# Optimization experiments

Measured on AMD Instinct MI355X. Metric: run time of the kernel, lower is better.

Reference implementation:

```python
import jax, jax.numpy as jnp
import numpy as np
import math

MASK_FILL = -1e6  # d2l masked_softmax fills masked scores with -1e6


def setup_inputs() -> dict:
    key = jax.random.key(0)
    kq, kk, kv, kl = jax.random.split(key, 4)
    B, Lq, Lk, D = 16, 2048, 2048, 64
    queries = jax.random.normal(kq, (B, Lq, D), dtype=jnp.float32)
    keys = jax.random.normal(kk, (B, Lk, D), dtype=jnp.float32)
    values = jax.random.normal(kv, (B, Lk, D), dtype=jnp.float32)
    valid_lens = jax.random.randint(kl, (B,), 1, Lk + 1, dtype=jnp.int32)
    return {"queries": queries, "keys": keys, "values": values, "valid_lens": valid_lens}


def reference(queries, keys, values, valid_lens):
    # scores: [B, Lq, Lk]
    d = queries.shape[-1]
    scores = jnp.einsum("bqd,bkd->bqk", queries, keys) / math.sqrt(d)
    # masked_softmax: positions >= valid_lens[b] along key axis get -1e6
    Lk = keys.shape[1]
    mask = jnp.arange(Lk)[None, None, :] < valid_lens[:, None, None]  # [B,1,Lk]
    scores = jnp.where(mask, scores, MASK_FILL)
    attn = jax.nn.softmax(scores, axis=-1)
    # dropout p=0.0 (eval) is identity
    return jnp.einsum("bqk,bkd->bqd", attn, values)
```

## Files before the change

kernel.cpp:

```cpp
#include <hip/hip_runtime.h>
#include <hip/hip_bf16.h>
#include <stdint.h>


#define BATCH 16
#define SEQ   2048
#define DIM   64
#define KBLK  32
#define QBLK  64
#define NSPLIT 2
#define NTHR  256

typedef __bf16 bf16x8 __attribute__((ext_vector_type(8)));
typedef float  f32x16 __attribute__((ext_vector_type(16)));
typedef unsigned int u32x2 __attribute__((ext_vector_type(2)));

static constexpr float QSCALE = 0.125f * 1.44269504088896340736f;

__device__ __forceinline__ uint32_t pk2bf(float a, float b) {
    union { __hip_bfloat162 h; uint32_t u; } c;
    c.h = __float22bfloat162_rn(make_float2(a, b));
    return c.u;
}
__device__ __forceinline__ bf16x8 mk8(uint32_t w0, uint32_t w1, uint32_t w2, uint32_t w3) {
    union { uint32_t u[4]; bf16x8 v; } c;
    c.u[0] = w0; c.u[1] = w1; c.u[2] = w2; c.u[3] = w3;
    return c.v;
}
__device__ __forceinline__ u32x2 plswap(uint32_t a, uint32_t b) {
    return __builtin_amdgcn_permlane32_swap(a, b, false, false);
}
__device__ __forceinline__ float vmax16(const f32x16& v) {
    float a = fmaxf(fmaxf(v[0], v[1]), fmaxf(v[2], v[3]));
    float b = fmaxf(fmaxf(v[4], v[5]), fmaxf(v[6], v[7]));
    float c = fmaxf(fmaxf(v[8], v[9]), fmaxf(v[10], v[11]));
    float d = fmaxf(fmaxf(v[12], v[13]), fmaxf(v[14], v[15]));
    return fmaxf(fmaxf(a, b), fmaxf(c, d));
}
__device__ __forceinline__ float vsum16(const f32x16& v) {
    float a = (v[0] + v[1]) + (v[2] + v[3]);
    float b = (v[4] + v[5]) + (v[6] + v[7]);
    float c = (v[8] + v[9]) + (v[10] + v[11]);
    float d = (v[12] + v[13]) + (v[14] + v[15]);
    return (a + b) + (c + d);
}

__global__ __launch_bounds__(256) void prep_kv(
        const float* __restrict__ K, const float* __restrict__ V,
        unsigned short* __restrict__ Kbf, unsigned short* __restrict__ Vt)
{
    __shared__ float tl[64][65];
    const int bid = blockIdx.x;
    const int b  = bid >> 5;
    const int kb = (bid & 31) * 64;
    const int tid = threadIdx.x;

    const float* Kp = K + ((size_t)b * SEQ + kb) * DIM;
    const float* Vp = V + ((size_t)b * SEQ + kb) * DIM;
    unsigned short* Ko = Kbf + ((size_t)b * SEQ + kb) * DIM;
    unsigned short* Vo = Vt + (size_t)b * SEQ * DIM + (size_t)(kb >> 5) * 2048;

    #pragma unroll
    for (int p = 0; p < 4; ++p) {
        int idx = p * 256 + tid;
        float4 x = ((const float4*)Kp)[idx];
        ((uint2*)Ko)[idx] = make_uint2(pk2bf(x.x, x.y), pk2bf(x.z, x.w));
    }
    #pragma unroll
    for (int p = 0; p < 4; ++p) {
        int idx = p * 256 + tid;
        int r = idx >> 4, c = (idx & 15) * 4;
        float4 x = *(const float4*)(Vp + r * DIM + c);
        tl[r][c] = x.x; tl[r][c+1] = x.y; tl[r][c+2] = x.z; tl[r][c+3] = x.w;
    }
    __syncthreads();
    #pragma unroll
    for (int p = 0; p < 4; ++p) {
        int idx = p * 256 + tid;
        int sub = idx >> 9;
        int rem = idx & 511;
        int d  = rem >> 3;
        int kq = (rem & 7) * 4;
        int kr = sub * 32 + kq;
        *(uint2*)(Vo + sub * 2048 + d * 32 + kq) =
            make_uint2(pk2bf(tl[kr][d],     tl[kr + 1][d]),
                       pk2bf(tl[kr + 2][d], tl[kr + 3][d]));
    }
}

__global__ __launch_bounds__(NTHR, 2) void attn_main(
        const float* __restrict__ Q, const unsigned short* __restrict__ Kbf,
        const unsigned short* __restrict__ Vt, const int* __restrict__ VL,
        float* __restrict__ O)
{
    __shared__ float comb[2][32 * 64 + 128];

    const int tid  = threadIdx.x;
    const int bid  = blockIdx.x;
    const int b    = bid >> 5;
    const int qt   = bid & 31;
    const int qb   = qt * QBLK;
    const int qhalf = (tid >> 6) & 1;
    const int split = tid >> 7;
    const int lane = tid & 63;
    const int h    = lane >> 5;
    const int ln   = lane & 31;

    const int valid  = VL[b];
    const int ntiles = (valid + KBLK - 1) / KBLK;

    const size_t bOff = (size_t)b * SEQ * DIM;
    const int qrow = qb + qhalf * 32 + ln;

    bf16x8 qf[4];
    {
        const float* qp = Q + bOff + (size_t)qrow * DIM;
        #pragma unroll
        for (int s = 0; s < 4; ++s) {
            int c0 = s * 16 + h * 8;
            float4 x = *(const float4*)(qp + c0);
            float4 y = *(const float4*)(qp + c0 + 4);
            qf[s] = mk8(pk2bf(x.x * QSCALE, x.y * QSCALE),
                        pk2bf(x.z * QSCALE, x.w * QSCALE),
                        pk2bf(y.x * QSCALE, y.y * QSCALE),
                        pk2bf(y.z * QSCALE, y.w * QSCALE));
        }
    }

    f32x16 o0, o1;
    #pragma unroll
    for (int r = 0; r < 16; ++r) { o0[r] = 0.0f; o1[r] = 0.0f; }
    float m_run = -1e30f, l_run = 0.0f;

    const unsigned short* kp  = Kbf + bOff + (size_t)ln * DIM + h * 8;
    const unsigned short* vpA = Vt + bOff + (size_t)ln * 32 + h * 8;

    bf16x8 ka[4], va[4];
    int kt = split;
    if (kt < ntiles) {
        const unsigned short* kq = kp + (size_t)kt * KBLK * DIM;
        #pragma unroll
        for (int s = 0; s < 4; ++s) ka[s] = *(const bf16x8*)(kq + s * 16);
        const unsigned short* vq = vpA + (size_t)kt * 2048;
        va[0] = *(const bf16x8*)(vq);
        va[1] = *(const bf16x8*)(vq + 16);
        va[2] = *(const bf16x8*)(vq + 1024);
        va[3] = *(const bf16x8*)(vq + 1024 + 16);
    }

    for (; kt < ntiles; kt += NSPLIT) {
        const int ktn = (kt + NSPLIT < ntiles) ? kt + NSPLIT : kt;
        bf16x8 kan[4], van[4];
        {
            const unsigned short* kq = kp + (size_t)ktn * KBLK * DIM;
            #pragma unroll
            for (int s = 0; s < 4; ++s) kan[s] = *(const bf16x8*)(kq + s * 16);
            const unsigned short* vq = vpA + (size_t)ktn * 2048;
            van[0] = *(const bf16x8*)(vq);
            van[1] = *(const bf16x8*)(vq + 16);
            van[2] = *(const bf16x8*)(vq + 1024);
            van[3] = *(const bf16x8*)(vq + 1024 + 16);
        }

        f32x16 st;
        #pragma unroll
        for (int r = 0; r < 16; ++r) st[r] = 0.0f;
        #pragma unroll
        for (int s = 0; s < 4; ++s)
            st = __builtin_amdgcn_mfma_f32_32x32x16_bf16(ka[s], qf[s], st, 0, 0, 0);

        const int kb = kt * KBLK;
        if (kb + KBLK > valid) {
            #pragma unroll
            for (int r = 0; r < 16; ++r) {
                int krel = (r & 3) + 8 * (r >> 2) + 4 * h;
                if (kb + krel >= valid) st[r] = -1e30f;
            }
        }

        float pm = vmax16(st);
        u32x2 sm = plswap(__float_as_uint(pm), __float_as_uint(pm));
        pm = fmaxf(__uint_as_float(sm[0]), __uint_as_float(sm[1]));
        if (!__all(pm <= m_run + 8.0f)) {
            float mnew = fmaxf(m_run, pm);
            float sc = __builtin_exp2f(m_run - mnew);
            l_run *= sc;
            #pragma unroll
            for (int r = 0; r < 16; ++r) { o0[r] *= sc; o1[r] *= sc; }
            m_run = mnew;
        }
        #pragma unroll
        for (int r = 0; r < 16; ++r) st[r] = __builtin_exp2f(st[r] - m_run);
        float ps = vsum16(st);
        u32x2 ss = plswap(__float_as_uint(ps), __float_as_uint(ps));
        l_run += __uint_as_float(ss[0]) + __uint_as_float(ss[1]);

        uint32_t W00 = pk2bf(st[0],  st[1]),  W01 = pk2bf(st[2],  st[3]);
        uint32_t W10 = pk2bf(st[4],  st[5]),  W11 = pk2bf(st[6],  st[7]);
        uint32_t W20 = pk2bf(st[8],  st[9]),  W21 = pk2bf(st[10], st[11]);
        uint32_t W30 = pk2bf(st[12], st[13]), W31 = pk2bf(st[14], st[15]);
        u32x2 sA = plswap(W00, W10), sB = plswap(W01, W11);
        bf16x8 bp0 = mk8(sA[0], sB[0], sA[1], sB[1]);
        u32x2 sC = plswap(W20, W30), sD = plswap(W21, W31);
        bf16x8 bp1 = mk8(sC[0], sD[0], sC[1], sD[1]);

        o0 = __builtin_amdgcn_mfma_f32_32x32x16_bf16(va[0], bp0, o0, 0, 0, 0);
        o0 = __builtin_amdgcn_mfma_f32_32x32x16_bf16(va[1], bp1, o0, 0, 0, 0);
        o1 = __builtin_amdgcn_mfma_f32_32x32x16_bf16(va[2], bp0, o1, 0, 0, 0);
        o1 = __builtin_amdgcn_mfma_f32_32x32x16_bf16(va[3], bp1, o1, 0, 0, 0);

        #pragma unroll
        for (int i = 0; i < 4; ++i) { ka[i] = kan[i]; va[i] = van[i]; }
    }

    float* base = comb[qhalf];
    if (split != 0) {
        #pragma unroll
        for (int r = 0; r < 16; ++r) {
            base[r * 64 + lane]        = o0[r];
            base[(r + 16) * 64 + lane] = o1[r];
        }
        base[2048 + lane]      = m_run;
        base[2048 + 64 + lane] = l_run;
    }
    __syncthreads();
    if (split == 0) {
        float mj = base[2048 + lane];
        float lj = base[2048 + 64 + lane];
        float M  = fmaxf(m_run, mj);
        float sc0 = __builtin_exp2f(m_run - M);
        float scj = __builtin_exp2f(mj - M);
        float lt = l_run * sc0 + lj * scj;
        float inv = 1.0f / lt;
        float* op = O + bOff + (size_t)qrow * DIM;
        #pragma unroll
        for (int a = 0; a < 4; ++a) {
            float4 w0, w1;
            w0.x = (o0[4*a+0]*sc0 + scj*base[(4*a+0)*64 + lane]) * inv;
            w0.y = (o0[4*a+1]*sc0 + scj*base[(4*a+1)*64 + lane]) * inv;
            w0.z = (o0[4*a+2]*sc0 + scj*base[(4*a+2)*64 + lane]) * inv;
            w0.w = (o0[4*a+3]*sc0 + scj*base[(4*a+3)*64 + lane]) * inv;
            w1.x = (o1[4*a+0]*sc0 + scj*base[(4*a+16)*64 + lane]) * inv;
            w1.y = (o1[4*a+1]*sc0 + scj*base[(4*a+17)*64 + lane]) * inv;
            w1.z = (o1[4*a+2]*sc0 + scj*base[(4*a+18)*64 + lane]) * inv;
            w1.w = (o1[4*a+3]*sc0 + scj*base[(4*a+19)*64 + lane]) * inv;
            *(float4*)(op + 8*a + 4*h)      = w0;
            *(float4*)(op + 32 + 8*a + 4*h) = w1;
        }
    }
}

__device__ __forceinline__ uint32_t swz(uint32_t row, uint32_t colByte) {
    return row * 128u + (colByte ^ ((row & 7u) << 4));
}
__device__ __forceinline__ bf16x8 lds8(const char* p) {
    union { uint4 q; bf16x8 v; } c;
    c.q = *(const uint4*)p;
    return c.v;
}

__global__ __launch_bounds__(256, 2) void attn_fallback(
        const float* __restrict__ Q, const float* __restrict__ K,
        const float* __restrict__ V, const int* __restrict__ VL,
        float* __restrict__ O)
{
    __shared__ unsigned short lds[2][2][64 * DIM];
    const int tid  = threadIdx.x;
    const int bid  = blockIdx.x;
    const int b    = bid & (BATCH - 1);
    const int qt   = bid >> 4;
    const int qb   = qt * 64;
    const int qhalf = (tid >> 6) & 1;
    const int split = tid >> 7;
    const int lane = tid & 63;
    const int h    = lane >> 5;
    const int ln   = lane & 31;
    const int ptid = tid & 127;

    const int valid  = VL[b];
    const int ntiles = (valid + 63) / 64;
    const int nit    = (ntiles + 1) / 2;

    const size_t bOff = (size_t)b * SEQ * DIM;
    const int qrow = qb + qhalf * 32 + ln;

    bf16x8 qf[4];
    {
        const float* qp = Q + bOff + (size_t)qrow * DIM;
        #pragma unroll
        for (int s = 0; s < 4; ++s) {
            int c0 = s * 16 + h * 8;
            float4 x = *(const float4*)(qp + c0);
            float4 y = *(const float4*)(qp + c0 + 4);
            qf[s] = mk8(pk2bf(x.x * QSCALE, x.y * QSCALE),
                        pk2bf(x.z * QSCALE, x.w * QSCALE),
                        pk2bf(y.x * QSCALE, y.y * QSCALE),
                        pk2bf(y.z * QSCALE, y.w * QSCALE));
        }
    }
    f32x16 o0, o1;
    #pragma unroll
    for (int r = 0; r < 16; ++r) { o0[r] = 0.0f; o1[r] = 0.0f; }
    float m_run = -1e30f, l_run = 0.0f;
    const float* Kb = K + bOff;
    const float* Vb = V + bOff;
    char* kls = (char*)lds[split][0];
    char* vls = (char*)lds[split][1];

    for (int it = 0; it < nit; ++it) {
        const int kt = it * 2 + split;
        const bool act = kt < ntiles;
        const int kb = kt * 64;
        if (act) {
            #pragma unroll
            for (int p = 0; p < 8; ++p) {
                int idx = p * 128 + ptid;
                int r = idx >> 4, c = (idx & 15) * 4;
                float4 kx = *(const float4*)(Kb + (size_t)(kb + r) * DIM + c);
                *(uint2*)(kls + swz(r, c * 2)) =
                    make_uint2(pk2bf(kx.x, kx.y), pk2bf(kx.z, kx.w));
            }
            #pragma unroll
            for (int p = 0; p < 2; ++p) {
                int idx = p * 128 + ptid;
                int cq = idx & 15, rq = idx >> 4;
                const float* vp = Vb + (size_t)(kb + rq * 4) * DIM + cq * 4;
                float4 v0 = *(const float4*)(vp);
                float4 v1 = *(const float4*)(vp + DIM);
                float4 v2 = *(const float4*)(vp + 2 * DIM);
                float4 v3 = *(const float4*)(vp + 3 * DIM);
// ... 48 lines not shown
            bf16x8 bp[4];
            {
                uint32_t u0 = pk2bf(st0[0], st0[1]),  u1 = pk2bf(st0[2], st0[3]);
                uint32_t u2 = pk2bf(st0[4], st0[5]),  u3 = pk2bf(st0[6], st0[7]);
                uint32_t u4 = pk2bf(st0[8], st0[9]),  u5 = pk2bf(st0[10], st0[11]);
                uint32_t u6 = pk2bf(st0[12], st0[13]), u7 = pk2bf(st0[14], st0[15]);
                u32x2 s02 = plswap(u0, u2), s13 = plswap(u1, u3);
                bp[0] = mk8(s02[0], s13[0], s02[1], s13[1]);
                u32x2 s46 = plswap(u4, u6), s57 = plswap(u5, u7);
                bp[1] = mk8(s46[0], s57[0], s46[1], s57[1]);
            }
            {
                uint32_t u0 = pk2bf(st1[0], st1[1]),  u1 = pk2bf(st1[2], st1[3]);
                uint32_t u2 = pk2bf(st1[4], st1[5]),  u3 = pk2bf(st1[6], st1[7]);
                uint32_t u4 = pk2bf(st1[8], st1[9]),  u5 = pk2bf(st1[10], st1[11]);
                uint32_t u6 = pk2bf(st1[12], st1[13]), u7 = pk2bf(st1[14], st1[15]);
                u32x2 s02 = plswap(u0, u2), s13 = plswap(u1, u3);
                bp[2] = mk8(s02[0], s13[0], s02[1], s13[1]);
                u32x2 s46 = plswap(u4, u6), s57 = plswap(u5, u7);
                bp[3] = mk8(s46[0], s57[0], s46[1], s57[1]);
            }
            #pragma unroll
            for (int x = 0; x < 4; ++x) {
                int cb = (x * 16 + h * 8) * 2;
                bf16x8 va0 = lds8(vls + swz(ln,      cb));
                bf16x8 va1 = lds8(vls + swz(ln + 32, cb));
                o0 = __builtin_amdgcn_mfma_f32_32x32x16_bf16(va0, bp[x], o0, 0, 0, 0);
                o1 = __builtin_amdgcn_mfma_f32_32x32x16_bf16(va1, bp[x], o1, 0, 0, 0);
            }
        }
        __syncthreads();
    }
    const int CSTRIDE = 32 * 64 + 128;
    float* comb = (float*)lds;
    if (split != 0) {
        float* base = comb + (size_t)qhalf * CSTRIDE;
        #pragma unroll
        for (int r = 0; r < 16; ++r) {
            base[r * 64 + lane]        = o0[r];
            base[(r + 16) * 64 + lane] = o1[r];
        }
        base[2048 + lane]      = m_run;
        base[2048 + 64 + lane] = l_run;
    }
    __syncthreads();
    if (split == 0) {
        float* base = comb + (size_t)qhalf * CSTRIDE;
        float mj = base[2048 + lane];
        float lj = base[2048 + 64 + lane];
        float M  = fmaxf(m_run, mj);
        float sc0 = __builtin_exp2f(m_run - M);
        float scj = __builtin_exp2f(mj - M);
        float lt = l_run * sc0 + lj * scj;
        float inv = 1.0f / lt;
        float* op = O + bOff + (size_t)qrow * DIM;
        #pragma unroll
        for (int a = 0; a < 4; ++a) {
            float4 w0, w1;
            w0.x = (o0[4*a+0]*sc0 + scj*base[(4*a+0)*64 + lane]) * inv;
            w0.y = (o0[4*a+1]*sc0 + scj*base[(4*a+1)*64 + lane]) * inv;
            w0.z = (o0[4*a+2]*sc0 + scj*base[(4*a+2)*64 + lane]) * inv;
            w0.w = (o0[4*a+3]*sc0 + scj*base[(4*a+3)*64 + lane]) * inv;
            w1.x = (o1[4*a+0]*sc0 + scj*base[(4*a+16)*64 + lane]) * inv;
            w1.y = (o1[4*a+1]*sc0 + scj*base[(4*a+17)*64 + lane]) * inv;
            w1.z = (o1[4*a+2]*sc0 + scj*base[(4*a+18)*64 + lane]) * inv;
            w1.w = (o1[4*a+3]*sc0 + scj*base[(4*a+19)*64 + lane]) * inv;
            *(float4*)(op + 8*a + 4*h)      = w0;
            *(float4*)(op + 32 + 8*a + 4*h) = w1;
        }
    }
}

extern "C" void kernel_launch(void* const* d_in, const int* in_sizes, int n_in,
                              void* d_out, int out_size, void* d_ws, size_t ws_size,
                              hipStream_t stream) {
    const float* q  = (const float*)d_in[0];
    const float* k  = (const float*)d_in[1];
    const float* v  = (const float*)d_in[2];
    const int*   vl = (const int*)d_in[3];
    float* out = (float*)d_out;

    const size_t KBYTES = (size_t)BATCH * SEQ * DIM * 2;
    if (ws_size >= 2 * KBYTES) {
        unsigned short* kbf = (unsigned short*)d_ws;
        unsigned short* vt  = (unsigned short*)((char*)d_ws + KBYTES);
        hipLaunchKernelGGL(prep_kv, dim3(BATCH * (SEQ / 64)), dim3(256), 0, stream,
                           k, v, kbf, vt);
        hipLaunchKernelGGL(attn_main, dim3(BATCH * (SEQ / QBLK)), dim3(NTHR), 0, stream,
                           q, kbf, vt, vl, out);
    } else {
        hipLaunchKernelGGL(attn_fallback, dim3(BATCH * (SEQ / 64)), dim3(256), 0, stream,
                           q, k, v, vl, out);
    }
}
```

Baseline: 47.85 us.

## Process two key tiles per iteration with MFMA priority and batch-interleaved block mapping

The main loop now handles 64 keys (two 32-key tiles) per iteration, so the online-softmax max/rescale and the reductions are done once per pair of tiles. V loads are issued at the top of each iteration and K for the next pair is prefetched after the QK MFMAs. The two MFMA groups are wrapped in s_setprio so waves doing matrix work get issue priority. Blocks are remapped so consecutive block IDs cycle across batches, spreading variable valid lengths more evenly over CUs. In exchange, register pressure rises from holding two score tiles plus eight V fragments, and V is no longer prefetched a full iteration ahead.

After: 52.16 us. +9.0%, slower.

```diff
diff --git a/kernel.cpp b/kernel.cpp
--- a/kernel.cpp
+++ b/kernel.cpp
@@ -6,7 +6,6 @@
 #define BATCH 16
 #define SEQ   2048
 #define DIM   64
-#define KBLK  32
 #define QBLK  64
 #define NSPLIT 2
 #define NTHR  256
@@ -97,8 +96,10 @@
 
     const int tid  = threadIdx.x;
     const int bid  = blockIdx.x;
-    const int b    = bid >> 5;
-    const int qt   = bid & 31;
+    const int half = bid >> 8;
+    const int r256 = bid & 255;
+    const int b    = ((r256 & 15) + half) & (BATCH - 1);
+    const int qt   = (r256 >> 4) + half * 16;
     const int qb   = qt * QBLK;
     const int qhalf = (tid >> 6) & 1;
     const int split = tid >> 7;
@@ -107,7 +108,7 @@
     const int ln   = lane & 31;
 
     const int valid  = VL[b];
-    const int ntiles = (valid + KBLK - 1) / KBLK;
+    const int npairs = (valid + 63) >> 6;
 
     const size_t bOff = (size_t)b * SEQ * DIM;
     const int qrow = qb + qhalf * 32 + ln;
@@ -135,50 +136,61 @@
     const unsigned short* kp  = Kbf + bOff + (size_t)ln * DIM + h * 8;
     const unsigned short* vpA = Vt + bOff + (size_t)ln * 32 + h * 8;
 
-    bf16x8 ka[4], va[4];
-    int kt = split;
-    if (kt < ntiles) {
-        const unsigned short* kq = kp + (size_t)kt * KBLK * DIM;
-        #pragma unroll
-        for (int s = 0; s < 4; ++s) ka[s] = *(const bf16x8*)(kq + s * 16);
-        const unsigned short* vq = vpA + (size_t)kt * 2048;
-        va[0] = *(const bf16x8*)(vq);
-        va[1] = *(const bf16x8*)(vq + 16);
-        va[2] = *(const bf16x8*)(vq + 1024);
-        va[3] = *(const bf16x8*)(vq + 1024 + 16);
-    }
-
-    for (; kt < ntiles; kt += NSPLIT) {
-        const int ktn = (kt + NSPLIT < ntiles) ? kt + NSPLIT : kt;
-        bf16x8 kan[4], van[4];
+    bf16x8 ka0[4], ka1[4];
+    int p = split;
+    if (p < npairs) {
+        const unsigned short* kq = kp + (size_t)p * 4096;
+        #pragma unroll
+        for (int s = 0; s < 4; ++s) {
+            ka0[s] = *(const bf16x8*)(kq + s * 16);
+            ka1[s] = *(const bf16x8*)(kq + 2048 + s * 16);
+        }
+    }
+
+    for (; p < npairs; p += NSPLIT) {
+        const unsigned short* vq = vpA + (size_t)p * 4096;
+        bf16x8 va00 = *(const bf16x8*)(vq);
+        bf16x8 va01 = *(const bf16x8*)(vq + 16);
+        bf16x8 va02 = *(const bf16x8*)(vq + 1024);
+        bf16x8 va03 = *(const bf16x8*)(vq + 1024 + 16);
+        bf16x8 va10 = *(const bf16x8*)(vq + 2048);
+        bf16x8 va11 = *(const bf16x8*)(vq + 2048 + 16);
+        bf16x8 va12 = *(const bf16x8*)(vq + 3072);
+        bf16x8 va13 = *(const bf16x8*)(vq + 3072 + 16);
+
+        f32x16 st0, st1;
+        #pragma unroll
+        for (int r = 0; r < 16; ++r) { st0[r] = 0.0f; st1[r] = 0.0f; }
+        __builtin_amdgcn_s_setprio(1);
+        #pragma unroll
+        for (int s = 0; s < 4; ++s) {
+            st0 = __builtin_amdgcn_mfma_f32_32x32x16_bf16(ka0[s], qf[s], st0, 0, 0, 0);
+            st1 = __builtin_amdgcn_mfma_f32_32x32x16_bf16(ka1[s], qf[s], st1, 0, 0, 0);
+        }
+        __builtin_amdgcn_s_setprio(0);
+
+        const int pn = (p + NSPLIT < npairs) ? p + NSPLIT : p;
+        bf16x8 kan0[4], kan1[4];
         {
-            const unsigned short* kq = kp + (size_t)ktn * KBLK * DIM;
-            #pragma unroll
-            for (int s = 0; s < 4; ++s) kan[s] = *(const bf16x8*)(kq + s * 16);
-            const unsigned short* vq = vpA + (size_t)ktn * 2048;
-            van[0] = *(const bf16x8*)(vq);
-            van[1] = *(const bf16x8*)(vq + 16);
-            van[2] = *(const bf16x8*)(vq + 1024);
-            van[3] = *(const bf16x8*)(vq + 1024 + 16);
-        }
-
-        f32x16 st;
-        #pragma unroll
-        for (int r = 0; r < 16; ++r) st[r] = 0.0f;
-        #pragma unroll
-        for (int s = 0; s < 4; ++s)
-            st = __builtin_amdgcn_mfma_f32_32x32x16_bf16(ka[s], qf[s], st, 0, 0, 0);
-
-        const int kb = kt * KBLK;
-        if (kb + KBLK > valid) {
+            const unsigned short* kqn = kp + (size_t)pn * 4096;
+            #pragma unroll
+            for (int s = 0; s < 4; ++s) {
+                kan0[s] = *(const bf16x8*)(kqn + s * 16);
+                kan1[s] = *(const bf16x8*)(kqn + 2048 + s * 16);
+            }
+        }
+
+        const int kb = p * 64;
+        if (kb + 64 > valid) {
             #pragma unroll
             for (int r = 0; r < 16; ++r) {
                 int krel = (r & 3) + 8 * (r >> 2) + 4 * h;
-                if (kb + krel >= valid) st[r] = -1e30f;
-            }
-        }
-
-        float pm = vmax16(st);
+                if (kb + krel      >= valid) st0[r] = -1e30f;
+                if (kb + 32 + krel >= valid) st1[r] = -1e30f;
+            }
+        }
+
+        float pm = fmaxf(vmax16(st0), vmax16(st1));
         u32x2 sm = plswap(__float_as_uint(pm), __float_as_uint(pm));
         pm = fmaxf(__uint_as_float(sm[0]), __uint_as_float(sm[1]));
         if (!__all(pm <= m_run + 8.0f)) {
@@ -190,27 +202,49 @@
             m_run = mnew;
         }
         #pragma unroll
-        for (int r = 0; r < 16; ++r) st[r] = __builtin_exp2f(st[r] - m_run);
-        float ps = vsum16(st);
+        for (int r = 0; r < 16; ++r) {
+            st0[r] = __builtin_exp2f(st0[r] - m_run);
+            st1[r] = __builtin_exp2f(st1[r] - m_run);
+        }
+        float ps = vsum16(st0) + vsum16(st1);
         u32x2 ss = plswap(__float_as_uint(ps), __float_as_uint(ps));
         l_run += __uint_as_float(ss[0]) + __uint_as_float(ss[1]);
 
-        uint32_t W00 = pk2bf(st[0],  st[1]),  W01 = pk2bf(st[2],  st[3]);
-        uint32_t W10 = pk2bf(st[4],  st[5]),  W11 = pk2bf(st[6],  st[7]);
-        uint32_t W20 = pk2bf(st[8],  st[9]),  W21 = pk2bf(st[10], st[11]);
-        uint32_t W30 = pk2bf(st[12], st[13]), W31 = pk2bf(st[14], st[15]);
-        u32x2 sA = plswap(W00, W10), sB = plswap(W01, W11);
-        bf16x8 bp0 = mk8(sA[0], sB[0], sA[1], sB[1]);
-        u32x2 sC = plswap(W20, W30), sD = plswap(W21, W31);
-        bf16x8 bp1 = mk8(sC[0], sD[0], sC[1], sD[1]);
-
-        o0 = __builtin_amdgcn_mfma_f32_32x32x16_bf16(va[0], bp0, o0, 0, 0, 0);
-        o0 = __builtin_amdgcn_mfma_f32_32x32x16_bf16(va[1], bp1, o0, 0, 0, 0);
-        o1 = __builtin_amdgcn_mfma_f32_32x32x16_bf16(va[2], bp0, o1, 0, 0, 0);
-        o1 = __builtin_amdgcn_mfma_f32_32x32x16_bf16(va[3], bp1, o1, 0, 0, 0);
-
-        #pragma unroll
-        for (int i = 0; i < 4; ++i) { ka[i] = kan[i]; va[i] = van[i]; }
+        bf16x8 bp00, bp01, bp10, bp11;
+        {
+            uint32_t u0 = pk2bf(st0[0],  st0[1]),  u1 = pk2bf(st0[2],  st0[3]);
+            uint32_t u2 = pk2bf(st0[4],  st0[5]),  u3 = pk2bf(st0[6],  st0[7]);
+            uint32_t u4 = pk2bf(st0[8],  st0[9]),  u5 = pk2bf(st0[10], st0[11]);
+            uint32_t u6 = pk2bf(st0[12], st0[13]), u7 = pk2bf(st0[14], st0[15]);
+            u32x2 sA = plswap(u0, u2), sB = plswap(u1, u3);
+            bp00 = mk8(sA[0], sB[0], sA[1], sB[1]);
+            u32x2 sC = plswap(u4, u6), sD = plswap(u5, u7);
+            bp01 = mk8(sC[0], sD[0], sC[1], sD[1]);
+        }
+        {
+            uint32_t u0 = pk2bf(st1[0],  st1[1]),  u1 = pk2bf(st1[2],  st1[3]);
+            uint32_t u2 = pk2bf(st1[4],  st1[5]),  u3 = pk2bf(st1[6],  st1[7]);
+            uint32_t u4 = pk2bf(st1[8],  st1[9]),  u5 = pk2bf(st1[10], st1[11]);
+            uint32_t u6 = pk2bf(st1[12], st1[13]), u7 = pk2bf(st1[14], st1[15]);
+            u32x2 sA = plswap(u0, u2), sB = plswap(u1, u3);
+            bp10 = mk8(sA[0], sB[0], sA[1], sB[1]);
+            u32x2 sC = plswap(u4, u6), sD = plswap(u5, u7);
+            bp11 = mk8(sC[0], sD[0], sC[1], sD[1]);
+        }
+
+        __builtin_amdgcn_s_setprio(1);
+        o0 = __builtin_amdgcn_mfma_f32_32x32x16_bf16(va00, bp00, o0, 0, 0, 0);
+        o1 = __builtin_amdgcn_mfma_f32_32x32x16_bf16(va02, bp00, o1, 0, 0, 0);
+        o0 = __builtin_amdgcn_mfma_f32_32x32x16_bf16(va01, bp01, o0, 0, 0, 0);
+        o1 = __builtin_amdgcn_mfma_f32_32x32x16_bf16(va03, bp01, o1, 0, 0, 0);
+        o0 = __builtin_amdgcn_mfma_f32_32x32x16_bf16(va10, bp10, o0, 0, 0, 0);
+        o1 = __builtin_amdgcn_mfma_f32_32x32x16_bf16(va12, bp10, o1, 0, 0, 0);
+        o0 = __builtin_amdgcn_mfma_f32_32x32x16_bf16(va11, bp11, o0, 0, 0, 0);
+        o1 = __builtin_amdgcn_mfma_f32_32x32x16_bf16(va13, bp11, o1, 0, 0, 0);
+        __builtin_amdgcn_s_setprio(0);
+
+        #pragma unroll
+        for (int i = 0; i < 4; ++i) { ka0[i] = kan0[i]; ka1[i] = kan1[i]; }
     }
 
     float* base = comb[qhalf];
```

## Have each wave process both 32-row query halves and split keys four ways

Applied to the files above, without the earlier changes.

Each wave now holds two 32-row query tiles (A and B) and reuses every loaded K/V fragment for both, so the per-wave global loads of K and V are amortised over twice the MFMA work. The key range is split across four waves instead of two, and the final reduction merges three partial results through a larger shared buffer. Block-to-batch mapping is also rotated to interleave batches across the grid, spreading uneven valid lengths. The cost is roughly doubled accumulator registers, which raises register pressure, plus a larger LDS combine step.

After: 42.37 us. 11.5% less time.

```diff
diff --git a/kernel.cpp b/kernel.cpp
--- a/kernel.cpp
+++ b/kernel.cpp
@@ -6,9 +6,7 @@
 #define BATCH 16
 #define SEQ   2048
 #define DIM   64
-#define KBLK  32
-#define QBLK  64
-#define NSPLIT 2
+#define NSPLIT 4
 #define NTHR  256
 
 typedef __bf16 bf16x8 __attribute__((ext_vector_type(8)));
@@ -93,55 +91,60 @@
         const unsigned short* __restrict__ Vt, const int* __restrict__ VL,
         float* __restrict__ O)
 {
-    __shared__ float comb[2][32 * 64 + 128];
+    __shared__ float comb[NSPLIT - 1][64 * 64 + 256];
 
     const int tid  = threadIdx.x;
-    const int bid  = blockIdx.x;
-    const int b    = bid >> 5;
-    const int qt   = bid & 31;
-    const int qb   = qt * QBLK;
-    const int qhalf = (tid >> 6) & 1;
-    const int split = tid >> 7;
+    const int idx  = blockIdx.x;
+    const int b    = ((idx & 15) + (idx >> 8)) & (BATCH - 1);
+    const int qt   = (idx >> 4) & 31;
+    const int qb   = qt * 64;
+    const int split = tid >> 6;
     const int lane = tid & 63;
     const int h    = lane >> 5;
     const int ln   = lane & 31;
 
     const int valid  = VL[b];
-    const int ntiles = (valid + KBLK - 1) / KBLK;
+    const int ntiles = (valid + 31) >> 5;
 
     const size_t bOff = (size_t)b * SEQ * DIM;
-    const int qrow = qb + qhalf * 32 + ln;
-
-    bf16x8 qf[4];
+
+    bf16x8 qfA[4], qfB[4];
     {
-        const float* qp = Q + bOff + (size_t)qrow * DIM;
+        const float* qpA = Q + bOff + (size_t)(qb + ln) * DIM;
+        const float* qpB = Q + bOff + (size_t)(qb + 32 + ln) * DIM;
         #pragma unroll
         for (int s = 0; s < 4; ++s) {
             int c0 = s * 16 + h * 8;
-            float4 x = *(const float4*)(qp + c0);
-            float4 y = *(const float4*)(qp + c0 + 4);
-            qf[s] = mk8(pk2bf(x.x * QSCALE, x.y * QSCALE),
-                        pk2bf(x.z * QSCALE, x.w * QSCALE),
-                        pk2bf(y.x * QSCALE, y.y * QSCALE),
-                        pk2bf(y.z * QSCALE, y.w * QSCALE));
-        }
-    }
-
-    f32x16 o0, o1;
+            float4 xa = *(const float4*)(qpA + c0);
+            float4 ya = *(const float4*)(qpA + c0 + 4);
+            qfA[s] = mk8(pk2bf(xa.x * QSCALE, xa.y * QSCALE),
+                         pk2bf(xa.z * QSCALE, xa.w * QSCALE),
+                         pk2bf(ya.x * QSCALE, ya.y * QSCALE),
+                         pk2bf(ya.z * QSCALE, ya.w * QSCALE));
+            float4 xb = *(const float4*)(qpB + c0);
+            float4 yb = *(const float4*)(qpB + c0 + 4);
+            qfB[s] = mk8(pk2bf(xb.x * QSCALE, xb.y * QSCALE),
+                         pk2bf(xb.z * QSCALE, xb.w * QSCALE),
+                         pk2bf(yb.x * QSCALE, yb.y * QSCALE),
+                         pk2bf(yb.z * QSCALE, yb.w * QSCALE));
+        }
+    }
+
+    f32x16 oA0, oA1, oB0, oB1;
     #pragma unroll
-    for (int r = 0; r < 16; ++r) { o0[r] = 0.0f; o1[r] = 0.0f; }
-    float m_run = -1e30f, l_run = 0.0f;
-
-    const unsigned short* kp  = Kbf + bOff + (size_t)ln * DIM + h * 8;
-    const unsigned short* vpA = Vt + bOff + (size_t)ln * 32 + h * 8;
+    for (int r = 0; r < 16; ++r) { oA0[r] = 0.0f; oA1[r] = 0.0f; oB0[r] = 0.0f; oB1[r] = 0.0f; }
+    float mA = -1e30f, lA = 0.0f, mB = -1e30f, lB = 0.0f;
+
+    const unsigned short* kp = Kbf + bOff + (size_t)ln * DIM + h * 8;
+    const unsigned short* vp = Vt  + bOff + (size_t)ln * 32  + h * 8;
 
     bf16x8 ka[4], va[4];
     int kt = split;
     if (kt < ntiles) {
-        const unsigned short* kq = kp + (size_t)kt * KBLK * DIM;
+        const unsigned short* kq = kp + (size_t)kt * 2048;
+        const unsigned short* vq = vp + (size_t)kt * 2048;
         #pragma unroll
         for (int s = 0; s < 4; ++s) ka[s] = *(const bf16x8*)(kq + s * 16);
-        const unsigned short* vq = vpA + (size_t)kt * 2048;
         va[0] = *(const bf16x8*)(vq);
         va[1] = *(const bf16x8*)(vq + 16);
         va[2] = *(const bf16x8*)(vq + 1024);
@@ -152,100 +155,168 @@
         const int ktn = (kt + NSPLIT < ntiles) ? kt + NSPLIT : kt;
         bf16x8 kan[4], van[4];
         {
-            const unsigned short* kq = kp + (size_t)ktn * KBLK * DIM;
+            const unsigned short* kq = kp + (size_t)ktn * 2048;
+            const unsigned short* vq = vp + (size_t)ktn * 2048;
             #pragma unroll
             for (int s = 0; s < 4; ++s) kan[s] = *(const bf16x8*)(kq + s * 16);
-            const unsigned short* vq = vpA + (size_t)ktn * 2048;
             van[0] = *(const bf16x8*)(vq);
             van[1] = *(const bf16x8*)(vq + 16);
             van[2] = *(const bf16x8*)(vq + 1024);
             van[3] = *(const bf16x8*)(vq + 1024 + 16);
         }
 
-        f32x16 st;
-        #pragma unroll
-        for (int r = 0; r < 16; ++r) st[r] = 0.0f;
-        #pragma unroll
-        for (int s = 0; s < 4; ++s)
-            st = __builtin_amdgcn_mfma_f32_32x32x16_bf16(ka[s], qf[s], st, 0, 0, 0);
-
-        const int kb = kt * KBLK;
-        if (kb + KBLK > valid) {
+        f32x16 stA, stB;
+        #pragma unroll
+        for (int r = 0; r < 16; ++r) { stA[r] = 0.0f; stB[r] = 0.0f; }
+        #pragma unroll
+        for (int s = 0; s < 4; ++s) {
+            stA = __builtin_amdgcn_mfma_f32_32x32x16_bf16(ka[s], qfA[s], stA, 0, 0, 0);
+            stB = __builtin_amdgcn_mfma_f32_32x32x16_bf16(ka[s], qfB[s], stB, 0, 0, 0);
+        }
+
+        const int kb = kt * 32;
+        if (kb + 32 > valid) {
             #pragma unroll
             for (int r = 0; r < 16; ++r) {
                 int krel = (r & 3) + 8 * (r >> 2) + 4 * h;
-                if (kb + krel >= valid) st[r] = -1e30f;
-            }
-        }
-
-        float pm = vmax16(st);
-        u32x2 sm = plswap(__float_as_uint(pm), __float_as_uint(pm));
-        pm = fmaxf(__uint_as_float(sm[0]), __uint_as_float(sm[1]));
-        if (!__all(pm <= m_run + 8.0f)) {
-            float mnew = fmaxf(m_run, pm);
-            float sc = __builtin_exp2f(m_run - mnew);
-            l_run *= sc;
-            #pragma unroll
-            for (int r = 0; r < 16; ++r) { o0[r] *= sc; o1[r] *= sc; }
-            m_run = mnew;
-        }
-        #pragma unroll
-        for (int r = 0; r < 16; ++r) st[r] = __builtin_exp2f(st[r] - m_run);
-        float ps = vsum16(st);
-        u32x2 ss = plswap(__float_as_uint(ps), __float_as_uint(ps));
-        l_run += __uint_as_float(ss[0]) + __uint_as_float(ss[1]);
-
-        uint32_t W00 = pk2bf(st[0],  st[1]),  W01 = pk2bf(st[2],  st[3]);
-        uint32_t W10 = pk2bf(st[4],  st[5]),  W11 = pk2bf(st[6],  st[7]);
-        uint32_t W20 = pk2bf(st[8],  st[9]),  W21 = pk2bf(st[10], st[11]);
-        uint32_t W30 = pk2bf(st[12], st[13]), W31 = pk2bf(st[14], st[15]);
-        u32x2 sA = plswap(W00, W10), sB = plswap(W01, W11);
-        bf16x8 bp0 = mk8(sA[0], sB[0], sA[1], sB[1]);
-        u32x2 sC = plswap(W20, W30), sD = plswap(W21, W31);
-        bf16x8 bp1 = mk8(sC[0], sD[0], sC[1], sD[1]);
-
-        o0 = __builtin_amdgcn_mfma_f32_32x32x16_bf16(va[0], bp0, o0, 0, 0, 0);
-        o0 = __builtin_amdgcn_mfma_f32_32x32x16_bf16(va[1], bp1, o0, 0, 0, 0);
-        o1 = __builtin_amdgcn_mfma_f32_32x32x16_bf16(va[2], bp0, o1, 0, 0, 0);
-        o1 = __builtin_amdgcn_mfma_f32_32x32x16_bf16(va[3], bp1, o1, 0, 0, 0);
+                if (kb + krel >= valid) { stA[r] = -1e30f; stB[r] = -1e30f; }
+            }
+        }
+
+        float pmA = vmax16(stA);
+        float pmB = vmax16(stB);
+        u32x2 smA = plswap(__float_as_uint(pmA), __float_as_uint(pmA));
+        u32x2 smB = plswap(__float_as_uint(pmB), __float_as_uint(pmB));
+        pmA = fmaxf(__uint_as_float(smA[0]), __uint_as_float(smA[1]));
+        pmB = fmaxf(__uint_as_float(smB[0]), __uint_as_float(smB[1]));
+        if (!__all(pmA <= mA + 8.0f)) {
+            float mn = fmaxf(mA, pmA);
+            float sc = __builtin_exp2f(mA - mn);
+            lA *= sc;
+            #pragma unroll
+            for (int r = 0; r < 16; ++r) { oA0[r] *= sc; oA1[r] *= sc; }
+            mA = mn;
+        }
+        if (!__all(pmB <= mB + 8.0f)) {
+            float mn = fmaxf(mB, pmB);
+            float sc = __builtin_exp2f(mB - mn);
+            lB *= sc;
+            #pragma unroll
+            for (int r = 0; r < 16; ++r) { oB0[r] *= sc; oB1[r] *= sc; }
+            mB = mn;
+        }
+        #pragma unroll
+        for (int r = 0; r < 16; ++r) {
+            stA[r] = __builtin_exp2f(stA[r] - mA);
+            stB[r] = __builtin_exp2f(stB[r] - mB);
+        }
+        float psA = vsum16(stA);
+        float psB = vsum16(stB);
+        u32x2 ssA = plswap(__float_as_uint(psA), __float_as_uint(psA));
+        u32x2 ssB = plswap(__float_as_uint(psB), __float_as_uint(psB));
+        lA += __uint_as_float(ssA[0]) + __uint_as_float(ssA[1]);
+        lB += __uint_as_float(ssB[0]) + __uint_as_float(ssB[1]);
+
+        bf16x8 bpA0, bpA1, bpB0, bpB1;
+        {
+            uint32_t u0 = pk2bf(stA[0],  stA[1]),  u1 = pk2bf(stA[2],  stA[3]);
+            uint32_t u2 = pk2bf(stA[4],  stA[5]),  u3 = pk2bf(stA[6],  stA[7]);
+            uint32_t u4 = pk2bf(stA[8],  stA[9]),  u5 = pk2bf(stA[10], stA[11]);
+            uint32_t u6 = pk2bf(stA[12], stA[13]), u7 = pk2bf(stA[14], stA[15]);
+            u32x2 sA = plswap(u0, u2), sB = plswap(u1, u3);
+            bpA0 = mk8(sA[0], sB[0], sA[1], sB[1]);
+            u32x2 sC = plswap(u4, u6), sD = plswap(u5, u7);
+            bpA1 = mk8(sC[0], sD[0], sC[1], sD[1]);
+        }
+        {
+            uint32_t u0 = pk2bf(stB[0],  stB[1]),  u1 = pk2bf(stB[2],  stB[3]);
+            uint32_t u2 = pk2bf(stB[4],  stB[5]),  u3 = pk2bf(stB[6],  stB[7]);
+            uint32_t u4 = pk2bf(stB[8],  stB[9]),  u5 = pk2bf(stB[10], stB[11]);
+            uint32_t u6 = pk2bf(stB[12], stB[13]), u7 = pk2bf(stB[14], stB[15]);
+            u32x2 sA = plswap(u0, u2), sB = plswap(u1, u3);
+            bpB0 = mk8(sA[0], sB[0], sA[1], sB[1]);
+            u32x2 sC = plswap(u4, u6), sD = plswap(u5, u7);
+            bpB1 = mk8(sC[0], sD[0], sC[1], sD[1]);
+        }
+
+        oA0 = __builtin_amdgcn_mfma_f32_32x32x16_bf16(va[0], bpA0, oA0, 0, 0, 0);
+        oB0 = __builtin_amdgcn_mfma_f32_32x32x16_bf16(va[0], bpB0, oB0, 0, 0, 0);
+        oA1 = __builtin_amdgcn_mfma_f32_32x32x16_bf16(va[2], bpA0, oA1, 0, 0, 0);
+        oB1 = __builtin_amdgcn_mfma_f32_32x32x16_bf16(va[2], bpB0, oB1, 0, 0, 0);
+        oA0 = __builtin_amdgcn_mfma_f32_32x32x16_bf16(va[1], bpA1, oA0, 0, 0, 0);
+        oB0 = __builtin_amdgcn_mfma_f32_32x32x16_bf16(va[1], bpB1, oB0, 0, 0, 0);
+        oA1 = __builtin_amdgcn_mfma_f32_32x32x16_bf16(va[3], bpA1, oA1, 0, 0, 0);
+        oB1 = __builtin_amdgcn_mfma_f32_32x32x16_bf16(va[3], bpB1, oB1, 0, 0, 0);
 
         #pragma unroll
         for (int i = 0; i < 4; ++i) { ka[i] = kan[i]; va[i] = van[i]; }
     }
 
-    float* base = comb[qhalf];
     if (split != 0) {
+        float* base = comb[split - 1];
         #pragma unroll
         for (int r = 0; r < 16; ++r) {
-            base[r * 64 + lane]        = o0[r];
-            base[(r + 16) * 64 + lane] = o1[r];
-        }
-        base[2048 + lane]      = m_run;
-        base[2048 + 64 + lane] = l_run;
+            base[r * 64 + lane]        = oA0[r];
+            base[(r + 16) * 64 + lane] = oA1[r];
+            base[(r + 32) * 64 + lane] = oB0[r];
+            base[(r + 48) * 64 + lane] = oB1[r];
+        }
+        base[4096 + lane]       = mA;
+        base[4096 + 64 + lane]  = lA;
+        base[4096 + 128 + lane] = mB;
+        base[4096 + 192 + lane] = lB;
     }
     __syncthreads();
     if (split == 0) {
-        float mj = base[2048 + lane];
-        float lj = base[2048 + 64 + lane];
-        float M  = fmaxf(m_run, mj);
-        float sc0 = __builtin_exp2f(m_run - M);
-        float scj = __builtin_exp2f(mj - M);
-        float lt = l_run * sc0 + lj * scj;
-        float inv = 1.0f / lt;
-        float* op = O + bOff + (size_t)qrow * DIM;
+        float MA = mA, MB = mB;
+        #pragma unroll
+        for (int j = 0; j < NSPLIT - 1; ++j) {
+            MA = fmaxf(MA, comb[j][4096 + lane]);
+            MB = fmaxf(MB, comb[j][4096 + 128 + lane]);
+        }
+        float scA = __builtin_exp2f(mA - MA), ltA = lA * scA;
+        float scB = __builtin_exp2f(mB - MB), ltB = lB * scB;
+        #pragma unroll
+        for (int r = 0; r < 16; ++r) {
+            oA0[r] *= scA; oA1[r] *= scA;
+            oB0[r] *= scB; oB1[r] *= scB;
+        }
+        #pragma unroll
+        for (int j = 0; j < NSPLIT - 1; ++j) {
+            float mjA = comb[j][4096 + lane];
+            float ljA = comb[j][4096 + 64 + lane];
+            float mjB = comb[j][4096 + 128 + lane];
+            float ljB = comb[j][4096 + 192 + lane];
+            float sjA = __builtin_exp2f(mjA - MA);
+            float sjB = __builtin_exp2f(mjB - MB);
+            ltA += ljA * sjA;
+            ltB += ljB * sjB;
+            #pragma unroll
+            for (int r = 0; r < 16; ++r) {
+                oA0[r] += sjA * comb[j][r * 64 + lane];
+                oA1[r] += sjA * comb[j][(r + 16) * 64 + lane];
+                oB0[r] += sjB * comb[j][(r + 32) * 64 + lane];
+                oB1[r] += sjB * comb[j][(r + 48) * 64 + lane];
+            }
+        }
+        float invA = 1.0f / ltA, invB = 1.0f / ltB;
+        float* opA = O + bOff + (size_t)(qb + ln) * DIM;
+        float* opB = O + bOff + (size_t)(qb + 32 + ln) * DIM;
         #pragma unroll
         for (int a = 0; a < 4; ++a) {
-            float4 w0, w1;
-            w0.x = (o0[4*a+0]*sc0 + scj*base[(4*a+0)*64 + lane]) * inv;
-            w0.y = (o0[4*a+1]*sc0 + scj*base[(4*a+1)*64 + lane]) * inv;
-            w0.z = (o0[4*a+2]*sc0 + scj*base[(4*a+2)*64 + lane]) * inv;
-            w0.w = (o0[4*a+3]*sc0 + scj*base[(4*a+3)*64 + lane]) * inv;
-            w1.x = (o1[4*a+0]*sc0 + scj*base[(4*a+16)*64 + lane]) * inv;
-            w1.y = (o1[4*a+1]*sc0 + scj*base[(4*a+17)*64 + lane]) * inv;
-            w1.z = (o1[4*a+2]*sc0 + scj*base[(4*a+18)*64 + lane]) * inv;
-            w1.w = (o1[4*a+3]*sc0 + scj*base[(4*a+19)*64 + lane]) * inv;
-            *(float4*)(op + 8*a + 4*h)      = w0;
-            *(float4*)(op + 32 + 8*a + 4*h) = w1;
+            float4 w;
+            w.x = oA0[4*a+0] * invA; w.y = oA0[4*a+1] * invA;
+            w.z = oA0[4*a+2] * invA; w.w = oA0[4*a+3] * invA;
+            *(float4*)(opA + 8*a + 4*h) = w;
+            w.x = oA1[4*a+0] * invA; w.y = oA1[4*a+1] * invA;
+            w.z = oA1[4*a+2] * invA; w.w = oA1[4*a+3] * invA;
+            *(float4*)(opA + 32 + 8*a + 4*h) = w;
+            w.x = oB0[4*a+0] * invB; w.y = oB0[4*a+1] * invB;
+            w.z = oB0[4*a+2] * invB; w.w = oB0[4*a+3] * invB;
+            *(float4*)(opB + 8*a + 4*h) = w;
+            w.x = oB1[4*a+0] * invB; w.y = oB1[4*a+1] * invB;
+            w.z = oB1[4*a+2] * invB; w.w = oB1[4*a+3] * invB;
+            *(float4*)(opB + 32 + 8*a + 4*h) = w;
         }
     }
 }
@@ -464,7 +535,7 @@
         unsigned short* vt  = (unsigned short*)((char*)d_ws + KBYTES);
         hipLaunchKernelGGL(prep_kv, dim3(BATCH * (SEQ / 64)), dim3(256), 0, stream,
                            k, v, kbf, vt);
-        hipLaunchKernelGGL(attn_main, dim3(BATCH * (SEQ / QBLK)), dim3(NTHR), 0, stream,
+        hipLaunchKernelGGL(attn_main, dim3(BATCH * (SEQ / 64)), dim3(NTHR), 0, stream,
                            q, kbf, vt, vl, out);
     } else {
         hipLaunchKernelGGL(attn_fallback, dim3(BATCH * (SEQ / 64)), dim3(256), 0, stream,
```

## Pre-swizzle K/V into lane-contiguous fragments, deepen prefetch, interleave batches across blocks

Applied to the files above, without the earlier changes.

The prep kernel now writes K and V in an MFMA-fragment layout, so each lane loads a contiguous 16-byte chunk per 1 KiB stripe and every load is fully coalesced. The main loop keeps four tile sets in registers in a rotating buffer, prefetching four tiles ahead, to hide global-memory latency. Block indices are remapped so consecutive blocks cover different batches, which spreads the uneven valid-length work across CUs. The costs are extra registers, which may hurt occupancy at launch bounds of 2, and an LDS transpose plus extra sync for K in the prep kernel.

New measurement: 90.51 us. 89.1% more time.

```diff
diff --git a/kernel.cpp b/kernel.cpp
--- a/kernel.cpp
+++ b/kernel.cpp
@@ -6,8 +6,6 @@
 #define BATCH 16
 #define SEQ   2048
 #define DIM   64
-#define KBLK  32
-#define QBLK  64
 #define NSPLIT 2
 #define NTHR  256
 
@@ -47,7 +45,7 @@
 
 __global__ __launch_bounds__(256) void prep_kv(
         const float* __restrict__ K, const float* __restrict__ V,
-        unsigned short* __restrict__ Kbf, unsigned short* __restrict__ Vt)
+        unsigned short* __restrict__ Kws, unsigned short* __restrict__ Vws)
 {
     __shared__ float tl[64][65];
     const int bid = blockIdx.x;
@@ -57,15 +55,33 @@
 
     const float* Kp = K + ((size_t)b * SEQ + kb) * DIM;
     const float* Vp = V + ((size_t)b * SEQ + kb) * DIM;
-    unsigned short* Ko = Kbf + ((size_t)b * SEQ + kb) * DIM;
-    unsigned short* Vo = Vt + (size_t)b * SEQ * DIM + (size_t)(kb >> 5) * 2048;
+    char* Ko = (char*)Kws + ((size_t)b * SEQ + kb) * DIM * 2;
+    char* Vo = (char*)Vws + ((size_t)b * SEQ + kb) * DIM * 2;
 
     #pragma unroll
     for (int p = 0; p < 4; ++p) {
         int idx = p * 256 + tid;
-        float4 x = ((const float4*)Kp)[idx];
-        ((uint2*)Ko)[idx] = make_uint2(pk2bf(x.x, x.y), pk2bf(x.z, x.w));
-    }
+        int r = idx >> 4, c = (idx & 15) * 4;
+        float4 x = *(const float4*)(Kp + r * DIM + c);
+        tl[r][c] = x.x; tl[r][c+1] = x.y; tl[r][c+2] = x.z; tl[r][c+3] = x.w;
+    }
+    __syncthreads();
+    #pragma unroll
+    for (int p = 0; p < 4; ++p) {
+        int idx = p * 256 + tid;
+        int o   = idx * 8;
+        int sub = o >> 12;
+        int rem = o & 4095;
+        int s   = rem >> 10;
+        int li  = (rem >> 4) & 63;
+        int h   = li >> 5, r = li & 31;
+        int e0  = (rem & 15) >> 1;
+        int d0  = s * 16 + h * 8 + e0;
+        int R   = sub * 32 + r;
+        *(uint2*)(Ko + o) = make_uint2(pk2bf(tl[R][d0],     tl[R][d0 + 1]),
+                                       pk2bf(tl[R][d0 + 2], tl[R][d0 + 3]));
+    }
+    __syncthreads();
     #pragma unroll
     for (int p = 0; p < 4; ++p) {
         int idx = p * 256 + tid;
@@ -77,29 +93,95 @@
     #pragma unroll
     for (int p = 0; p < 4; ++p) {
         int idx = p * 256 + tid;
-        int sub = idx >> 9;
-        int rem = idx & 511;
-        int d  = rem >> 3;
-        int kq = (rem & 7) * 4;
-        int kr = sub * 32 + kq;
-        *(uint2*)(Vo + sub * 2048 + d * 32 + kq) =
-            make_uint2(pk2bf(tl[kr][d],     tl[kr + 1][d]),
-                       pk2bf(tl[kr + 2][d], tl[kr + 3][d]));
-    }
-}
+        int o   = idx * 8;
+        int sub = o >> 12;
+        int rem = o & 4095;
+        int f   = rem >> 10;
+        int li  = (rem >> 4) & 63;
+        int hh  = li >> 5, ln = li & 31;
+        int e0  = (rem & 15) >> 1;
+        int kk0 = (f & 1) * 16 + hh * 8 + e0;
+        int d   = (f >> 1) * 32 + ln;
+        int K0  = sub * 32 + kk0;
+        *(uint2*)(Vo + o) = make_uint2(pk2bf(tl[K0][d],     tl[K0 + 1][d]),
+                                       pk2bf(tl[K0 + 2][d], tl[K0 + 3][d]));
+    }
+}
+
+#define LOADSET(KA, VA, T) do {                                              \
+    const char* kq_ = kgl + (size_t)(T) * 4096;                              \
+    const char* vq_ = vgl + (size_t)(T) * 4096;                              \
+    KA[0] = *(const bf16x8*)(kq_);          KA[1] = *(const bf16x8*)(kq_ + 1024); \
+    KA[2] = *(const bf16x8*)(kq_ + 2048);   KA[3] = *(const bf16x8*)(kq_ + 3072); \
+    VA[0] = *(const bf16x8*)(vq_);          VA[1] = *(const bf16x8*)(vq_ + 1024); \
+    VA[2] = *(const bf16x8*)(vq_ + 2048);   VA[3] = *(const bf16x8*)(vq_ + 3072); \
+} while (0)
+
+#define BODY(KA, VA) do {                                                    \
+    f32x16 st;                                                               \
+    _Pragma("unroll")                                                        \
+    for (int r = 0; r < 16; ++r) st[r] = 0.0f;                               \
+    _Pragma("unroll")                                                        \
+    for (int s = 0; s < 4; ++s)                                              \
+        st = __builtin_amdgcn_mfma_f32_32x32x16_bf16(KA[s], qf[s], st, 0, 0, 0); \
+    int pf_ = kt + 4 * NSPLIT;                                               \
+    if (pf_ >= ntiles) pf_ = kt;                                             \
+    {   const char* kq_ = kgl + (size_t)pf_ * 4096;                          \
+        KA[0] = *(const bf16x8*)(kq_);        KA[1] = *(const bf16x8*)(kq_ + 1024); \
+        KA[2] = *(const bf16x8*)(kq_ + 2048); KA[3] = *(const bf16x8*)(kq_ + 3072); } \
+    const int kb_ = kt * 32;                                                 \
+    if (kb_ + 32 > valid) {                                                  \
+        _Pragma("unroll")                                                    \
+        for (int r = 0; r < 16; ++r) {                                       \
+            int krel = (r & 3) + 8 * (r >> 2) + 4 * h;                       \
+            if (kb_ + krel >= valid) st[r] = -1e30f;                         \
+        }                                                                    \
+    }                                                                        \
+    float pm = vmax16(st);                                                   \
+    u32x2 sm = plswap(__float_as_uint(pm), __float_as_uint(pm));             \
+    pm = fmaxf(__uint_as_float(sm[0]), __uint_as_float(sm[1]));              \
+    if (!__all(pm <= m_run + 8.0f)) {                                        \
+        float mnew = fmaxf(m_run, pm);                                       \
+        float sc = __builtin_exp2f(m_run - mnew);                            \
+        l_run *= sc;                                                         \
+        _Pragma("unroll")                                                    \
+        for (int r = 0; r < 16; ++r) { o0[r] *= sc; o1[r] *= sc; }           \
+        m_run = mnew;                                                        \
+    }                                                                        \
+    _Pragma("unroll")                                                        \
+    for (int r = 0; r < 16; ++r) st[r] = __builtin_exp2f(st[r] - m_run);     \
+    float ps = vsum16(st);                                                   \
+    u32x2 ss = plswap(__float_as_uint(ps), __float_as_uint(ps));             \
+    l_run += __uint_as_float(ss[0]) + __uint_as_float(ss[1]);                \
+    uint32_t W00 = pk2bf(st[0],  st[1]),  W01 = pk2bf(st[2],  st[3]);        \
+    uint32_t W10 = pk2bf(st[4],  st[5]),  W11 = pk2bf(st[6],  st[7]);        \
+    uint32_t W20 = pk2bf(st[8],  st[9]),  W21 = pk2bf(st[10], st[11]);       \
+    uint32_t W30 = pk2bf(st[12], st[13]), W31 = pk2bf(st[14], st[15]);       \
+    u32x2 sA = plswap(W00, W10), sB = plswap(W01, W11);                      \
+    bf16x8 bp0 = mk8(sA[0], sB[0], sA[1], sB[1]);                            \
+    u32x2 sC = plswap(W20, W30), sD = plswap(W21, W31);                      \
+    bf16x8 bp1 = mk8(sC[0], sD[0], sC[1], sD[1]);                            \
+    o0 = __builtin_amdgcn_mfma_f32_32x32x16_bf16(VA[0], bp0, o0, 0, 0, 0);   \
+    o1 = __builtin_amdgcn_mfma_f32_32x32x16_bf16(VA[2], bp0, o1, 0, 0, 0);   \
+    o0 = __builtin_amdgcn_mfma_f32_32x32x16_bf16(VA[1], bp1, o0, 0, 0, 0);   \
+    o1 = __builtin_amdgcn_mfma_f32_32x32x16_bf16(VA[3], bp1, o1, 0, 0, 0);   \
+    {   const char* vq_ = vgl + (size_t)pf_ * 4096;                          \
+        VA[0] = *(const bf16x8*)(vq_);        VA[1] = *(const bf16x8*)(vq_ + 1024); \
+        VA[2] = *(const bf16x8*)(vq_ + 2048); VA[3] = *(const bf16x8*)(vq_ + 3072); } \
+} while (0)
 
 __global__ __launch_bounds__(NTHR, 2) void attn_main(
-        const float* __restrict__ Q, const unsigned short* __restrict__ Kbf,
-        const unsigned short* __restrict__ Vt, const int* __restrict__ VL,
+        const float* __restrict__ Q, const unsigned short* __restrict__ Kws,
+        const unsigned short* __restrict__ Vws, const int* __restrict__ VL,
         float* __restrict__ O)
 {
     __shared__ float comb[2][32 * 64 + 128];
 
     const int tid  = threadIdx.x;
-    const int bid  = blockIdx.x;
-    const int b    = bid >> 5;
-    const int qt   = bid & 31;
-    const int qb   = qt * QBLK;
+    const int idx  = blockIdx.x;
+    const int b    = ((idx & 15) + (idx >> 8)) & (BATCH - 1);
+    const int qt   = (idx >> 4) & 31;
+    const int qb   = qt * 64;
     const int qhalf = (tid >> 6) & 1;
     const int split = tid >> 7;
     const int lane = tid & 63;
@@ -107,7 +189,7 @@
     const int ln   = lane & 31;
 
     const int valid  = VL[b];
-    const int ntiles = (valid + KBLK - 1) / KBLK;
+    const int ntiles = (valid + 31) >> 5;
 
     const size_t bOff = (size_t)b * SEQ * DIM;
     const int qrow = qb + qhalf * 32 + ln;
@@ -132,85 +214,26 @@
     for (int r = 0; r < 16; ++r) { o0[r] = 0.0f; o1[r] = 0.0f; }
     float m_run = -1e30f, l_run = 0.0f;
 
-    const unsigned short* kp  = Kbf + bOff + (size_t)ln * DIM + h * 8;
-    const unsigned short* vpA = Vt + bOff + (size_t)ln * 32 + h * 8;
-
-    bf16x8 ka[4], va[4];
+    const char* kgl = (const char*)Kws + bOff * 2 + (size_t)lane * 16;
+    const char* vgl = (const char*)Vws + bOff * 2 + (size_t)lane * 16;
+
+    bf16x8 K0[4], V0[4], K1[4], V1[4], K2[4], V2[4], K3[4], V3[4];
     int kt = split;
     if (kt < ntiles) {
-        const unsigned short* kq = kp + (size_t)kt * KBLK * DIM;
-        #pragma unroll
-        for (int s = 0; s < 4; ++s) ka[s] = *(const bf16x8*)(kq + s * 16);
-        const unsigned short* vq = vpA + (size_t)kt * 2048;
-        va[0] = *(const bf16x8*)(vq);
-        va[1] = *(const bf16x8*)(vq + 16);
-        va[2] = *(const bf16x8*)(vq + 1024);
-        va[3] = *(const bf16x8*)(vq + 1024 + 16);
-    }
-
-    for (; kt < ntiles; kt += NSPLIT) {
-        const int ktn = (kt + NSPLIT < ntiles) ? kt + NSPLIT : kt;
-        bf16x8 kan[4], van[4];
-        {
-            const unsigned short* kq = kp + (size_t)ktn * KBLK * DIM;
-            #pragma unroll
-            for (int s = 0; s < 4; ++s) kan[s] = *(const bf16x8*)(kq + s * 16);
-            const unsigned short* vq = vpA + (size_t)ktn * 2048;
-            van[0] = *(const bf16x8*)(vq);
-            van[1] = *(const bf16x8*)(vq + 16);
-            van[2] = *(const bf16x8*)(vq + 1024);
-            van[3] = *(const bf16x8*)(vq + 1024 + 16);
-        }
-
-        f32x16 st;
-        #pragma unroll
-        for (int r = 0; r < 16; ++r) st[r] = 0.0f;
-        #pragma unroll
-        for (int s = 0; s < 4; ++s)
-            st = __builtin_amdgcn_mfma_f32_32x32x16_bf16(ka[s], qf[s], st, 0, 0, 0);
-
-        const int kb = kt * KBLK;
-        if (kb + KBLK > valid) {
-            #pragma unroll
-            for (int r = 0; r < 16; ++r) {
-                int krel = (r & 3) + 8 * (r >> 2) + 4 * h;
-                if (kb + krel >= valid) st[r] = -1e30f;
-            }
-        }
-
-        float pm = vmax16(st);
-        u32x2 sm = plswap(__float_as_uint(pm), __float_as_uint(pm));
-        pm = fmaxf(__uint_as_float(sm[0]), __uint_as_float(sm[1]));
-        if (!__all(pm <= m_run + 8.0f)) {
-            float mnew = fmaxf(m_run, pm);
-            float sc = __builtin_exp2f(m_run - mnew);
-            l_run *= sc;
-            #pragma unroll
-            for (int r = 0; r < 16; ++r) { o0[r] *= sc; o1[r] *= sc; }
-            m_run = mnew;
-        }
-        #pragma unroll
-        for (int r = 0; r < 16; ++r) st[r] = __builtin_exp2f(st[r] - m_run);
-        float ps = vsum16(st);
-        u32x2 ss = plswap(__float_as_uint(ps), __float_as_uint(ps));
-        l_run += __uint_as_float(ss[0]) + __uint_as_float(ss[1]);
-
-        uint32_t W00 = pk2bf(st[0],  st[1]),  W01 = pk2bf(st[2],  st[3]);
-        uint32_t W10 = pk2bf(st[4],  st[5]),  W11 = pk2bf(st[6],  st[7]);
-        uint32_t W20 = pk2bf(st[8],  st[9]),  W21 = pk2bf(st[10], st[11]);
-        uint32_t W30 = pk2bf(st[12], st[13]), W31 = pk2bf(st[14], st[15]);
-        u32x2 sA = plswap(W00, W10), sB = plswap(W01, W11);
-        bf16x8 bp0 = mk8(sA[0], sB[0], sA[1], sB[1]);
-        u32x2 sC = plswap(W20, W30), sD = plswap(W21, W31);
-        bf16x8 bp1 = mk8(sC[0], sD[0], sC[1], sD[1]);
-
-        o0 = __builtin_amdgcn_mfma_f32_32x32x16_bf16(va[0], bp0, o0, 0, 0, 0);
-        o0 = __builtin_amdgcn_mfma_f32_32x32x16_bf16(va[1], bp1, o0, 0, 0, 0);
-        o1 = __builtin_amdgcn_mfma_f32_32x32x16_bf16(va[2], bp0, o1, 0, 0, 0);
-        o1 = __builtin_amdgcn_mfma_f32_32x32x16_bf16(va[3], bp1, o1, 0, 0, 0);
-
-        #pragma unroll
-        for (int i = 0; i < 4; ++i) { ka[i] = kan[i]; va[i] = van[i]; }
+        int t0 = kt;
+        int t1 = (kt + 1 * NSPLIT < ntiles) ? kt + 1 * NSPLIT : kt;
+        int t2 = (kt + 2 * NSPLIT < ntiles) ? kt + 2 * NSPLIT : kt;
+        int t3 = (kt + 3 * NSPLIT < ntiles) ? kt + 3 * NSPLIT : kt;
+        LOADSET(K0, V0, t0);
+        LOADSET(K1, V1, t1);
+        LOADSET(K2, V2, t2);
+        LOADSET(K3, V3, t3);
+        for (;;) {
+            BODY(K0, V0); kt += NSPLIT; if (kt >= ntiles) break;
+            BODY(K1, V1); kt += NSPLIT; if (kt >= ntiles) break;
+            BODY(K2, V2); kt += NSPLIT; if (kt >= ntiles) break;
+            BODY(K3, V3); kt += NSPLIT; if (kt >= ntiles) break;
+        }
     }
 
     float* base = comb[qhalf];
@@ -460,12 +483,12 @@
 
     const size_t KBYTES = (size_t)BATCH * SEQ * DIM * 2;
     if (ws_size >= 2 * KBYTES) {
-        unsigned short* kbf = (unsigned short*)d_ws;
-        unsigned short* vt  = (unsigned short*)((char*)d_ws + KBYTES);
+        unsigned short* kws = (unsigned short*)d_ws;
+        unsigned short* vws = (unsigned short*)((char*)d_ws + KBYTES);
         hipLaunchKernelGGL(prep_kv, dim3(BATCH * (SEQ / 64)), dim3(256), 0, stream,
-                           k, v, kbf, vt);
-        hipLaunchKernelGGL(attn_main, dim3(BATCH * (SEQ / QBLK)), dim3(NTHR), 0, stream,
-                           q, kbf, vt, vl, out);
+                           k, v, kws, vws);
+        hipLaunchKernelGGL(attn_main, dim3(BATCH * (SEQ / 64)), dim3(NTHR), 0, stream,
+                           q, kws, vws, vl, out);
     } else {
         hipLaunchKernelGGL(attn_fallback, dim3(BATCH * (SEQ / 64)), dim3(256), 0, stream,
                            q, k, v, vl, out);
```
